# Performance work log

Hardware: AMD Instinct MI355X
Metric: run time of the kernel (lower is better)

Reference implementation:

```python
import jax, jax.numpy as jnp
import numpy as np

C, H, V, N, T = 256, 256, 10000, 8, 256


def _residual_mlp(x, w1, b1, w2, b2, w3, b3):
    # ResidualLayerOld: relu(lin2(relu(lin1(x)))) + x, then final Linear
    h = jax.nn.relu(x @ w1 + b1)
    h = jax.nn.relu(h @ w2 + b2) + x
    return h @ w3 + b3


def setup_inputs() -> dict:
    key = jax.random.key(0)
    ks = jax.random.split(key, 16)
    p = lambda k, shape: jax.random.normal(k, shape, jnp.float32) * 0.02
    return dict(
        text=jax.random.randint(ks[0], (N, T), 0, V),
        mask=jnp.ones((N, T), dtype=bool),
        lengths=jnp.full((N,), T - 1, dtype=jnp.int32),  # full-length sequences
        start_emb=jax.random.normal(ks[1], (C, H), jnp.float32),
        state_emb=jax.random.normal(ks[2], (C, H), jnp.float32),
        preterminal_emb=jax.random.normal(ks[3], (C, H), jnp.float32),
        start_w1=p(ks[4], (H, H)), start_b1=jnp.zeros((H,), jnp.float32),
        start_w2=p(ks[5], (H, H)), start_b2=jnp.zeros((H,), jnp.float32),
        start_w3=p(ks[6], (H, 1)), start_b3=jnp.zeros((1,), jnp.float32),
        trans_w1=p(ks[7], (H, H)), trans_b1=jnp.zeros((H,), jnp.float32),
        trans_w2=p(ks[8], (H, H)), trans_b2=jnp.zeros((H,), jnp.float32),
        trans_w3=p(ks[9], (H, C)), trans_b3=jnp.zeros((C,), jnp.float32),
        term_w1=p(ks[10], (H, H)), term_b1=jnp.zeros((H,), jnp.float32),
        term_w2=p(ks[11], (H, H)), term_b2=jnp.zeros((H,), jnp.float32),
        term_w3=p(ks[12], (H, V)), term_b3=jnp.zeros((V,), jnp.float32),
    )


def _score(text, mask, lengths,
           start_emb, state_emb, preterminal_emb,
           start_w1, start_b1, start_w2, start_b2, start_w3, start_b3,
           trans_w1, trans_b1, trans_w2, trans_b2, trans_w3, trans_b3,
           term_w1, term_b1, term_w2, term_b2, term_w3, term_b3):
    n, t = text.shape
    c = state_emb.shape[0]
    # start / transition / emission distributions (dropout_type == 'none')
    init = jax.nn.log_softmax(
        _residual_mlp(start_emb, start_w1, start_b1, start_w2, start_b2, start_w3, start_b3)[:, 0], -1)  # [C]
    trans = jax.nn.log_softmax(
        _residual_mlp(state_emb, trans_w1, trans_b1, trans_w2, trans_b2, trans_w3, trans_b3), -1)  # [C,C]
    log_em = jax.nn.log_softmax(
        _residual_mlp(preterminal_emb, term_w1, term_b1, term_w2, term_b2, term_w3, term_b3), -1)  # [C,V]
    obs = log_em.T[text]  # [N,T,C], log p(x_t | z=c)
    # torch_struct LinearChain.hmm edge potentials: phi[n,t,c_next,c_prev]
    phi = trans[None, None] + obs[:, 1:, :, None]  # [N,T-1,C,C]
    phi = phi.at[:, 0].add(init[None, None, :] + obs[:, 0][:, None, :])
    phi_t = jnp.swapaxes(phi, 0, 1)  # [T-1,N,C,C]

    def fwd_step(alpha, p):
        new = jax.nn.logsumexp(p + alpha[:, None, :], axis=-1)  # reduce over c_prev
        return new, new

    _, alphas = jax.lax.scan(fwd_step, jnp.zeros((n, c), phi.dtype), phi_t)  # [T-1,N,C]

    def bwd_step(beta, p):
        new = jax.nn.logsumexp(p + beta[:, :, None], axis=1)  # reduce over c_next
        return new, beta

    _, betas = jax.lax.scan(bwd_step, jnp.zeros((n, c), phi.dtype), phi_t, reverse=True)  # [T-1,N,C]

    alpha_prev = jnp.concatenate([jnp.zeros((1, n, c), phi.dtype), alphas[:-1]], 0)
    log_Z = jax.nn.logsumexp(alphas[-1], -1)  # [N]
    # edge posteriors
    log_m = alpha_prev[:, :, None, :] + phi_t + betas[:, :, :, None] - log_Z[None, :, None, None]
    marginals = jnp.swapaxes(jnp.exp(log_m), 0, 1)  # [N,T-1,C,C]

    evidence = jax.nn.logsumexp(alphas[lengths - 1, jnp.arange(n)], -1).sum()
    elbo = jnp.where(mask[:, 1:, None, None],
                     jax.lax.stop_gradient(marginals) * phi,
                     0.0).sum()
    return elbo, evidence


def reference(text, mask, lengths,
              start_emb, state_emb, preterminal_emb,
              start_w1, start_b1, start_w2, start_b2, start_w3, start_b3,
              trans_w1, trans_b1, trans_w2, trans_b2, trans_w3, trans_b3,
              term_w1, term_b1, term_w2, term_b2, term_w3, term_b3):
    elbo, evidence = _score(text, mask, lengths,
                            start_emb, state_emb, preterminal_emb,
                            start_w1, start_b1, start_w2, start_b2, start_w3, start_b3,
                            trans_w1, trans_b1, trans_w2, trans_b2, trans_w3, trans_b3,
                            term_w1, term_b1, term_w2, term_b2, term_w3, term_b3)
    return elbo, evidence
```

## Files before the change

kernel.cpp:

```cpp
#include <hip/hip_runtime.h>
#include <hip/hip_bf16.h>

#define C_ 256
#define H_ 256
#define V_ 10000
#define N_ 8
#define T_ 256
#define TM1_ 255
#define NB_ ((V_ + 31) / 32)
#define SW_ 8

typedef _Float16 h2_t __attribute__((ext_vector_type(2)));
typedef _Float16 h4_t __attribute__((ext_vector_type(4)));
typedef _Float16 h8_t __attribute__((ext_vector_type(8)));
typedef float f4v __attribute__((ext_vector_type(4)));

__device__ __forceinline__ void bar_lgkm() {
  asm volatile("s_waitcnt lgkmcnt(0)\ns_barrier" ::: "memory");
}

__device__ __forceinline__ float wave_red_max(float v) {
#define DPP_MAX(ctrl) { int iv_ = __float_as_int(v); \
  int r_ = __builtin_amdgcn_update_dpp(iv_, iv_, ctrl, 0xF, 0xF, false); \
  v = fmaxf(v, __int_as_float(r_)); }
// ... 37 lines not shown
  const int tid = threadIdx.x;
#pragma unroll
  for (int rr = 0; rr < 4; ++rr)
    e_s[rr][tid] = emb[(r0 + rr) * H_ + tid];
  __syncthreads();
  float bb = b1[tid];
  float a0 = bb, a1 = bb, a2 = bb, a3 = bb;
  for (int k4 = 0; k4 < H_ / 4; ++k4) {
    float4 e0 = ((const float4*)e_s[0])[k4];
    float4 e1 = ((const float4*)e_s[1])[k4];
    float4 e2 = ((const float4*)e_s[2])[k4];
    float4 e3 = ((const float4*)e_s[3])[k4];
    const float* wp = w1 + (k4 * 4) * H_ + tid;
    float wa = wp[0], wb = wp[H_], wc = wp[2 * H_], wd = wp[3 * H_];
    a0 = fmaf(e0.x, wa, a0); a0 = fmaf(e0.y, wb, a0);
    a0 = fmaf(e0.z, wc, a0); a0 = fmaf(e0.w, wd, a0);
    a1 = fmaf(e1.x, wa, a1); a1 = fmaf(e1.y, wb, a1);
    a1 = fmaf(e1.z, wc, a1); a1 = fmaf(e1.w, wd, a1);
    a2 = fmaf(e2.x, wa, a2); a2 = fmaf(e2.y, wb, a2);
    a2 = fmaf(e2.z, wc, a2); a2 = fmaf(e2.w, wd, a2);
    a3 = fmaf(e3.x, wa, a3); a3 = fmaf(e3.y, wb, a3);
    a3 = fmaf(e3.z, wc, a3); a3 = fmaf(e3.w, wd, a3);
  }
  h_s[0][tid] = fmaxf(a0, 0.f);
  h_s[1][tid] = fmaxf(a1, 0.f);
  h_s[2][tid] = fmaxf(a2, 0.f);
  h_s[3][tid] = fmaxf(a3, 0.f);
  __syncthreads();
  bb = b2[tid];
  a0 = bb; a1 = bb; a2 = bb; a3 = bb;
  for (int k4 = 0; k4 < H_ / 4; ++k4) {
    float4 e0 = ((const float4*)h_s[0])[k4];
    float4 e1 = ((const float4*)h_s[1])[k4];
    float4 e2 = ((const float4*)h_s[2])[k4];
    float4 e3 = ((const float4*)h_s[3])[k4];
    const float* wp = w2 + (k4 * 4) * H_ + tid;
    float wa = wp[0], wb = wp[H_], wc = wp[2 * H_], wd = wp[3 * H_];
    a0 = fmaf(e0.x, wa, a0); a0 = fmaf(e0.y, wb, a0);
    a0 = fmaf(e0.z, wc, a0); a0 = fmaf(e0.w, wd, a0);
    a1 = fmaf(e1.x, wa, a1); a1 = fmaf(e1.y, wb, a1);
    a1 = fmaf(e1.z, wc, a1); a1 = fmaf(e1.w, wd, a1);
    a2 = fmaf(e2.x, wa, a2); a2 = fmaf(e2.y, wb, a2);
    a2 = fmaf(e2.z, wc, a2); a2 = fmaf(e2.w, wd, a2);
    a3 = fmaf(e3.x, wa, a3); a3 = fmaf(e3.y, wb, a3);
    a3 = fmaf(e3.z, wc, a3); a3 = fmaf(e3.w, wd, a3);
  }
  h2_s[0][tid] = fmaxf(a0, 0.f) + e_s[0][tid];
  h2_s[1][tid] = fmaxf(a1, 0.f) + e_s[1][tid];
  h2_s[2][tid] = fmaxf(a2, 0.f) + e_s[2][tid];
  h2_s[3][tid] = fmaxf(a3, 0.f) + e_s[3][tid];
  __syncthreads();
}

__global__ __launch_bounds__(256) void k_start(
    const float* __restrict__ emb, const float* __restrict__ w1,
    const float* __restrict__ b1, const float* __restrict__ w2,
    const float* __restrict__ b2, const float* __restrict__ w3,
    const float* __restrict__ b3, float* __restrict__ slogit) {
  __shared__ __align__(16) float e_s[4][C_], h_s[4][C_], h2_s[4][C_];
  __shared__ float red[4];
  const int r0 = blockIdx.x * 4;
  const int tid = threadIdx.x;
  mlp4(emb, w1, b1, w2, b2, r0, e_s, h_s, h2_s);
  float w3v = w3[tid];
  float s0 = block_allsum(h2_s[0][tid] * w3v, red);
  float s1 = block_allsum(h2_s[1][tid] * w3v, red);
  float s2 = block_allsum(h2_s[2][tid] * w3v, red);
  float s3 = block_allsum(h2_s[3][tid] * w3v, red);
  if (tid == 0) {
    float bb = b3[0];
    slogit[r0 + 0] = s0 + bb;
    slogit[r0 + 1] = s1 + bb;
    slogit[r0 + 2] = s2 + bb;
    slogit[r0 + 3] = s3 + bb;
  }
}

__global__ void k_init(const float* __restrict__ slogit, float* __restrict__ initv) {
  __shared__ float red[4];
  const int tid = threadIdx.x;
  float x = slogit[tid];
  float m = block_allmax(x, red);
  float se = block_allsum(__expf(x - m), red);
  initv[tid] = x - m - __logf(se);
}

__global__ __launch_bounds__(256) void k_trans(
    const float* __restrict__ emb, const float* __restrict__ w1,
    const float* __restrict__ b1, const float* __restrict__ w2,
    const float* __restrict__ b2, const float* __restrict__ w3,
    const float* __restrict__ b3, float* __restrict__ Pf,
    float* __restrict__ PLf, float* __restrict__ PTf,
    _Float16* __restrict__ P_h, _Float16* __restrict__ PT_h) {
  __shared__ __align__(16) float e_s[4][C_], h_s[4][C_], h2_s[4][C_];
  __shared__ float red[4];
  const int r0 = blockIdx.x * 4;
  const int tid = threadIdx.x;
  mlp4(emb, w1, b1, w2, b2, r0, e_s, h_s, h2_s);
  float lb = b3[tid];
  float l0 = lb, l1 = lb, l2 = lb, l3 = lb;
  for (int k4 = 0; k4 < H_ / 4; ++k4) {
    float4 e0 = ((const float4*)h2_s[0])[k4];
    float4 e1 = ((const float4*)h2_s[1])[k4];
    float4 e2 = ((const float4*)h2_s[2])[k4];
    float4 e3 = ((const float4*)h2_s[3])[k4];
    const float* wp = w3 + (k4 * 4) * C_ + tid;
    float wa = wp[0], wb = wp[C_], wc = wp[2 * C_], wd = wp[3 * C_];
    l0 = fmaf(e0.x, wa, l0); l0 = fmaf(e0.y, wb, l0);
    l0 = fmaf(e0.z, wc, l0); l0 = fmaf(e0.w, wd, l0);
    l1 = fmaf(e1.x, wa, l1); l1 = fmaf(e1.y, wb, l1);
    l1 = fmaf(e1.z, wc, l1); l1 = fmaf(e1.w, wd, l1);
    l2 = fmaf(e2.x, wa, l2); l2 = fmaf(e2.y, wb, l2);
    l2 = fmaf(e2.z, wc, l2); l2 = fmaf(e2.w, wd, l2);
    l3 = fmaf(e3.x, wa, l3); l3 = fmaf(e3.y, wb, l3);
    l3 = fmaf(e3.z, wc, l3); l3 = fmaf(e3.w, wd, l3);
  }
  float lg[4] = {l0, l1, l2, l3};
#pragma unroll
  for (int rr = 0; rr < 4; ++rr) {
    float m = block_allmax(lg[rr], red);
    float e = __expf(lg[rr] - m);
    float se = block_allsum(e, red);
    float p = e / se;
    float tv = lg[rr] - m - __logf(se);
    const int r = r0 + rr;
    Pf[r * C_ + tid] = p;
    PLf[r * C_ + tid] = p * tv;
    PTf[tid * C_ + r] = p;
    P_h[r * C_ + tid] = (_Float16)p;
    PT_h[tid * C_ + r] = (_Float16)p;
  }
}

__global__ __launch_bounds__(256) void k_term_mlp(
    const float* __restrict__ emb, const float* __restrict__ w1,
    const float* __restrict__ b1, const float* __restrict__ w2,
    const float* __restrict__ b2, float* __restrict__ H2,
    float* __restrict__ H2T) {
  __shared__ __align__(16) float e_s[4][C_], h_s[4][C_], h2_s[4][C_];
  const int r0 = blockIdx.x * 4;
  const int tid = threadIdx.x;
  mlp4(emb, w1, b1, w2, b2, r0, e_s, h_s, h2_s);
#pragma unroll
  for (int rr = 0; rr < 4; ++rr) {
    const int r = r0 + rr;
    float v = h2_s[rr][tid];
    H2[r * H_ + tid] = v;
    H2T[tid * C_ + r] = v;
  }
}

__global__ __launch_bounds__(256) void k_term_stats(
    const float* __restrict__ H2, const float* __restrict__ w3,
    const float* __restrict__ b3, float* __restrict__ partm,
    float* __restrict__ parts) {
  __shared__ __align__(16) float w3_s[H_][32];
  __shared__ float b3_s[32];
  const int v0 = blockIdx.x * 32;
  const int tid = threadIdx.x;
  const int ncols = min(32, V_ - v0);
  for (int idx = tid; idx < H_ * 32; idx += 256) {
    int k = idx >> 5, c = idx & 31;
    w3_s[k][c] = (c < ncols) ? w3[k * V_ + v0 + c] : 0.f;
  }
  if (tid < 32) b3_s[tid] = (tid < ncols) ? b3[v0 + tid] : 0.f;
  __syncthreads();
  float acc[32];
#pragma unroll
  for (int c = 0; c < 32; ++c) acc[c] = 0.f;
  const float4* hq = (const float4*)(H2 + tid * H_);
  for (int k4 = 0; k4 < H_ / 4; ++k4) {
    float4 h = hq[k4];
    float hk[4];
    *(float4*)hk = h;
#pragma unroll
    for (int kk = 0; kk < 4; ++kk) {
      float hv = hk[kk];
      const int k = k4 * 4 + kk;
      const float4* wq = (const float4*)(&w3_s[k][0]);
#pragma unroll
      for (int c4 = 0; c4 < 8; ++c4) {
        float4 w = wq[c4];
        acc[c4 * 4 + 0] = fmaf(hv, w.x, acc[c4 * 4 + 0]);
        acc[c4 * 4 + 1] = fmaf(hv, w.y, acc[c4 * 4 + 1]);
        acc[c4 * 4 + 2] = fmaf(hv, w.z, acc[c4 * 4 + 2]);
        acc[c4 * 4 + 3] = fmaf(hv, w.w, acc[c4 * 4 + 3]);
      }
    }
  }
  float m = -1e30f;
#pragma unroll
  for (int c = 0; c < 32; ++c) {
    acc[c] += b3_s[c];
    if (c < ncols) m = fmaxf(m, acc[c]);
  }
  float se = 0.f;
#pragma unroll
  for (int c = 0; c < 32; ++c)
    if (c < ncols) se += __expf(acc[c] - m);
  partm[blockIdx.x * C_ + tid] = m;
  parts[blockIdx.x * C_ + tid] = se;
}

__global__ void k_denom(const float* __restrict__ partm,
                        const float* __restrict__ parts,
                        float* __restrict__ denom) {
  const int r = threadIdx.x;
  float m = -1e30f;
  for (int b = 0; b < NB_; ++b) m = fmaxf(m, partm[b * C_ + r]);
  float s = 0.f;
  for (int b = 0; b < NB_; ++b)
    s += parts[b * C_ + r] * __expf(partm[b * C_ + r] - m);
  denom[r] = m + __logf(s);
}

__global__ __launch_bounds__(256) void k_obs2(
    const int* __restrict__ text, const float* __restrict__ H2T,
    const float* __restrict__ w3, const float* __restrict__ b3,
    const float* __restrict__ denom, float* __restrict__ EOBS,
    float* __restrict__ Karr) {
  __shared__ __align__(16) float w_s[H_][8];
  __shared__ float redm[4][8];
  const int c = threadIdx.x;
  const int wid = c >> 6;
  const int lane = c & 63;
  const int base = blockIdx.x * 8;
  int tok[8];
#pragma unroll
  for (int i = 0; i < 8; ++i) tok[i] = text[base + i];
  float wtmp[8];
#pragma unroll
  for (int i = 0; i < 8; ++i) wtmp[i] = w3[c * V_ + tok[i]];
  float b3t[8];
#pragma unroll
  for (int i = 0; i < 8; ++i) b3t[i] = b3[tok[i]];
#pragma unroll
  for (int i = 0; i < 8; ++i) w_s[c][i] = wtmp[i];
  __syncthreads();
  float acc[8];
#pragma unroll
  for (int i = 0; i < 8; ++i) acc[i] = 0.f;
  for (int k4 = 0; k4 < H_ / 4; ++k4) {
    float hv[4];
#pragma unroll
    for (int kk = 0; kk < 4; ++kk) hv[kk] = H2T[(k4 * 4 + kk) * C_ + c];
#pragma unroll
    for (int kk = 0; kk < 4; ++kk) {
      const float4* wq = (const float4*)(&w_s[k4 * 4 + kk][0]);
      float4 wa = wq[0], wb = wq[1];
      acc[0] = fmaf(hv[kk], wa.x, acc[0]);
      acc[1] = fmaf(hv[kk], wa.y, acc[1]);
      acc[2] = fmaf(hv[kk], wa.z, acc[2]);
      acc[3] = fmaf(hv[kk], wa.w, acc[3]);
      acc[4] = fmaf(hv[kk], wb.x, acc[4]);
      acc[5] = fmaf(hv[kk], wb.y, acc[5]);
      acc[6] = fmaf(hv[kk], wb.z, acc[6]);
      acc[7] = fmaf(hv[kk], wb.w, acc[7]);
    }
  }
  float dn = denom[c];
  float obsv[8];
#pragma unroll
  for (int i = 0; i < 8; ++i) obsv[i] = acc[i] + b3t[i] - dn;
#pragma unroll
  for (int i = 0; i < 8; ++i) {
    float wm = wave_red_max(obsv[i]);
    if (lane == 0) redm[wid][i] = wm;
  }
  __syncthreads();
#pragma unroll
  for (int i = 0; i < 8; ++i) {
    float Ki = fmaxf(fmaxf(redm[0][i], redm[1][i]),
                     fmaxf(redm[2][i], redm[3][i]));
    EOBS[(base + i) * C_ + c] = __expf(obsv[i] - Ki);
    if (c == 0) Karr[base + i] = Ki;
  }
}

__global__ __launch_bounds__(512, 2) void k_scan5(
    const _Float16* __restrict__ P_h, const _Float16* __restrict__ PT_h,
    const float* __restrict__ initv, const float* __restrict__ EOBS,
    const float* __restrict__ Karr, float* __restrict__ AL,
    float* __restrict__ BL, float* __restrict__ CC, float* __restrict__ DD,
    float* __restrict__ LOGZ) {
  __shared__ __align__(16) _Float16 ubuf[2][C_];
  __shared__ __align__(16) float red[SW_];
  const int tid = threadIdx.x;
  const int w = tid >> 6;
  const int lane = tid & 63;
  const int quad = lane >> 4;
  const int nn16 = lane & 15;
  const bool bwd = blockIdx.x >= N_;
  const int n = blockIdx.x & (N_ - 1);
  const _Float16* __restrict__ M = bwd ? PT_h : P_h;

  h8_t afrag[2][8];
#pragma unroll
  for (int m = 0; m < 2; ++m) {
    const _Float16* rp = M + (size_t)((w << 5) + (m << 4) + nn16) * C_ + (quad << 3);
#pragma unroll
    for (int kt = 0; kt < 8; ++kt)
      afrag[m][kt] = *(const h8_t*)(rp + (kt << 5));
  }
  const int stb = (w << 5) + (quad << 2);

  if (!bwd) {
    float K0 = Karr[n * T_];
    f4v x0[2];
    float lmax = -1e30f;
#pragma unroll
    for (int m = 0; m < 2; ++m) {
      const int st0 = stb + (m << 4);
      f4v iv = *(const f4v*)(initv + st0);
      f4v e0 = *(const f4v*)(EOBS + (size_t)(n * T_) * C_ + st0);
#pragma unroll
      for (int r = 0; r < 4; ++r) {
        x0[m][r] = iv[r] + __logf(e0[r]) + K0;
        lmax = fmaxf(lmax, x0[m][r]);
      }
    }
    float wmx = wave_red_max(lmax);
    if (lane == 0) red[w] = wmx;
    __syncthreads();
    f4v rr0 = *(const f4v*)&red[0];
    f4v rr1 = *(const f4v*)&red[4];
    float m0 = fmaxf(fmaxf(fmaxf(rr0[0], rr0[1]), fmaxf(rr0[2], rr0[3])),
                     fmaxf(fmaxf(rr1[0], rr1[1]), fmaxf(rr1[2], rr1[3])));
    __syncthreads();
    float Cacc = m0;
    f4v uval[2];
#pragma unroll
    for (int m = 0; m < 2; ++m) {
      const int st0 = stb + (m << 4);
#pragma unroll
      for (int r = 0; r < 4; ++r) uval[m][r] = __expf(x0[m][r] - m0);
      if (nn16 == 0) {
        h4_t p;
#pragma unroll
        for (int r = 0; r < 4; ++r) p[r] = (_Float16)uval[m][r];
        *(h4_t*)(&ubuf[0][st0]) = p;
        *(f4v*)(AL + (size_t)(0 * N_ + n) * C_ + st0) = uval[m];
      }
    }
    if (tid == 0) CC[0 * N_ + n] = Cacc;
    float invm = 1.f, logm = 0.f;
    f4v eo_nx[2], eo_p1[2];
#pragma unroll
    for (int m = 0; m < 2; ++m) {
      eo_nx[m] = *(const f4v*)(EOBS + (size_t)(n * T_ + 1) * C_ + stb + (m << 4));
      eo_p1[m] = *(const f4v*)(EOBS + (size_t)(n * T_ + 2) * C_ + stb + (m << 4));
    }
    float K_nx = Karr[n * T_ + 1];
    float K_p1 = Karr[n * T_ + 2];
    __syncthreads();

#pragma unroll 1
    for (int t = 0; t < TM1_; ++t) {
      const int cur = t & 1, nxt = cur ^ 1;
      f4v eo_p2[2];
      float K_p2 = 0.f;
      if (t + 3 < T_) {
#pragma unroll
        for (int m = 0; m < 2; ++m)
          eo_p2[m] = *(const f4v*)(EOBS + (size_t)(n * T_ + t + 3) * C_ + stb + (m << 4));
        K_p2 = Karr[n * T_ + t + 3];
      }
      h8_t bf[8];
#pragma unroll
      for (int kt = 0; kt < 8; ++kt)
        bf[kt] = *(const h8_t*)(&ubuf[cur][(kt << 5) + (quad << 3)]);
      f4v acc[2];
      acc[0] = (f4v){0.f, 0.f, 0.f, 0.f};
      acc[1] = (f4v){0.f, 0.f, 0.f, 0.f};
#pragma unroll
      for (int kt = 0; kt < 8; ++kt) {
        acc[0] = __builtin_amdgcn_mfma_f32_16x16x32_f16(afrag[0][kt], bf[kt], acc[0], 0, 0, 0);
        acc[1] = __builtin_amdgcn_mfma_f32_16x16x32_f16(afrag[1][kt], bf[kt], acc[1], 0, 0, 0);
      }
      float lmx = -1e30f;
#pragma unroll
      for (int m = 0; m < 2; ++m) {
#pragma unroll
        for (int r = 0; r < 4; ++r) {
          float u = acc[m][r] * invm * eo_nx[m][r];
          uval[m][r] = u;
          lmx = fmaxf(lmx, u);
        }
      }
      Cacc += K_nx + logm;
      const bool resc = (t & 3) == 3;
      if (resc) {
        float wmm = wave_red_max(lmx);
        if (lane == 0) red[w] = wmm;
      }
      if (nn16 == 0) {
#pragma unroll
        for (int m = 0; m < 2; ++m) {
          const int st0 = stb + (m << 4);
          h4_t p;
#pragma unroll
          for (int r = 0; r < 4; ++r) p[r] = (_Float16)uval[m][r];
          *(h4_t*)(&ubuf[nxt][st0]) = p;
          *(f4v*)(AL + (size_t)((t + 1) * N_ + n) * C_ + st0) = uval[m];
        }
      }
      if (tid == 0) CC[(t + 1) * N_ + n] = Cacc;
      bar_lgkm();
      if (resc) {
        f4v q0 = *(const f4v*)&red[0];
        f4v q1 = *(const f4v*)&red[4];
        float mm = fmaxf(fmaxf(fmaxf(q0[0], q0[1]), fmaxf(q0[2], q0[3])),
                         fmaxf(fmaxf(q1[0], q1[1]), fmaxf(q1[2], q1[3])));
        mm = fmaxf(mm, 1e-30f);
        invm = 1.f / mm;
        logm = __logf(mm);
      } else { invm = 1.f; logm = 0.f; }
#pragma unroll
      for (int m = 0; m < 2; ++m) { eo_nx[m] = eo_p1[m]; eo_p1[m] = eo_p2[m]; }
      K_nx = K_p1; K_p1 = K_p2;
    }
    float s = 0.f;
#pragma unroll
    for (int m = 0; m < 2; ++m)
      s += (uval[m][0] + uval[m][1]) + (uval[m][2] + uval[m][3]);
    s = wave_red_sum(s);
    if (lane == 0) red[w] = s;
    __syncthreads();
    if (tid == 0) {
      float S = ((red[0] + red[1]) + (red[2] + red[3])) +
                ((red[4] + red[5]) + (red[6] + red[7]));
      LOGZ[n] = __logf(S * (1.f / 16.f)) + Cacc;
    }
  } else {
    float Dacc = 0.f;
    f4v vval[2];
#pragma unroll
    for (int m = 0; m < 2; ++m) {
      const int st0 = stb + (m << 4);
      vval[m] = *(const f4v*)(EOBS + ((size_t)n * T_ + TM1_) * C_ + st0);
      if (nn16 == 0) {
        h4_t p;
#pragma unroll
        for (int r = 0; r < 4; ++r) p[r] = (_Float16)vval[m][r];
        *(h4_t*)(&ubuf[0][st0]) = p;
        f4v one = (f4v){1.f, 1.f, 1.f, 1.f};
        *(f4v*)(BL + (size_t)((TM1_ - 1) * N_ + n) * C_ + st0) = one;
      }
    }
    if (tid == 0) DD[(TM1_ - 1) * N_ + n] = 0.f;
    float K_nx = Karr[n * T_ + TM1_];
    float K_p1 = Karr[n * T_ + TM1_ - 1];
    f4v eo_nx[2], eo_p1[2];
#pragma unroll
    for (int m = 0; m < 2; ++m) {
      eo_nx[m] = *(const f4v*)(EOBS + (size_t)(n * T_ + TM1_ - 1) * C_ + stb + (m << 4));
      eo_p1[m] = *(const f4v*)(EOBS + (size_t)(n * T_ + TM1_ - 2) * C_ + stb + (m << 4));
    }
    float invm = 1.f, logm = 0.f;
    __syncthreads();

#pragma unroll 1
    for (int it = 0, t = TM1_ - 2; t >= 0; --t, ++it) {
      const int cur = it & 1, nxt = cur ^ 1;
      f4v eo_p2[2];
      float K_p2 = 0.f;
      if (t >= 2) {
#pragma unroll
        for (int m = 0; m < 2; ++m)
          eo_p2[m] = *(const f4v*)(EOBS + (size_t)(n * T_ + t - 1) * C_ + stb + (m << 4));
        K_p2 = Karr[n * T_ + t];
      }
      h8_t bf[8];
#pragma unroll
      for (int kt = 0; kt < 8; ++kt)
        bf[kt] = *(const h8_t*)(&ubuf[cur][(kt << 5) + (quad << 3)]);
      f4v acc[2];
      acc[0] = (f4v){0.f, 0.f, 0.f, 0.f};
      acc[1] = (f4v){0.f, 0.f, 0.f, 0.f};
#pragma unroll
      for (int kt = 0; kt < 8; ++kt) {
        acc[0] = __builtin_amdgcn_mfma_f32_16x16x32_f16(afrag[0][kt], bf[kt], acc[0], 0, 0, 0);
        acc[1] = __builtin_amdgcn_mfma_f32_16x16x32_f16(afrag[1][kt], bf[kt], acc[1], 0, 0, 0);
      }
      Dacc += K_nx + logm;
      float lmx = -1e30f;
      f4v blv[2];
#pragma unroll
      for (int m = 0; m < 2; ++m) {
#pragma unroll
        for (int r = 0; r < 4; ++r) {
          float b = acc[m][r] * invm;
          blv[m][r] = b;
          float v = b * eo_nx[m][r];
          vval[m][r] = v;
          lmx = fmaxf(lmx, v);
        }
      }
      if (((it + 1) & 3) == 3) {
        float wmm = wave_red_max(lmx);
        if (lane == 0) red[w] = wmm;
      }
      if (nn16 == 0) {
#pragma unroll
        for (int m = 0; m < 2; ++m) {
          const int st0 = stb + (m << 4);
          h4_t p;
#pragma unroll
          for (int r = 0; r < 4; ++r) p[r] = (_Float16)vval[m][r];
          *(h4_t*)(&ubuf[nxt][st0]) = p;
          *(f4v*)(BL + (size_t)(t * N_ + n) * C_ + st0) = blv[m];
        }
      }
      if (tid == 0) DD[t * N_ + n] = Dacc;
      bar_lgkm();
      if (((it + 1) & 3) == 3) {
        f4v q0 = *(const f4v*)&red[0];
        f4v q1 = *(const f4v*)&red[4];
        float mm = fmaxf(fmaxf(fmaxf(q0[0], q0[1]), fmaxf(q0[2], q0[3])),
                         fmaxf(fmaxf(q1[0], q1[1]), fmaxf(q1[2], q1[3])));
        mm = fmaxf(mm, 1e-30f);
        invm = 1.f / mm;
        logm = __logf(mm);
      } else { invm = 1.f; logm = 0.f; }
#pragma unroll
      for (int m = 0; m < 2; ++m) { eo_nx[m] = eo_p1[m]; eo_p1[m] = eo_p2[m]; }
      K_nx = K_p1; K_p1 = K_p2;
    }
  }
}

__global__ __launch_bounds__(256) void k_elbo(
    const float* __restrict__ Pf, const float* __restrict__ PLf,
    const float* __restrict__ PTf, const float* __restrict__ AL,
    const float* __restrict__ BL, const float* __restrict__ CC,
    const float* __restrict__ DD, const float* __restrict__ EOBS,
    const float* __restrict__ Karr, const float* __restrict__ LOGZ,
    float* __restrict__ out) {
  __shared__ __align__(16) float A_s[N_][C_];
  __shared__ __align__(16) float B_s[N_][C_];
  __shared__ float red[4];
  const int t = blockIdx.x;
  const int c = threadIdx.x;
  if (t == 0 && c == 0) {
    float s = 0.f;
#pragma unroll
    for (int nn = 0; nn < N_; ++nn) s += LOGZ[nn];
    out[1] = s;
  }
  float sc[N_], Kv[N_], cc[N_];
#pragma unroll
  for (int nn = 0; nn < N_; ++nn) {
    A_s[nn][c] = AL[(t * N_ + nn) * C_ + c];
    Kv[nn] = Karr[nn * T_ + t + 1];
    cc[nn] = CC[t * N_ + nn];
    sc[nn] = __expf(cc[nn] + DD[t * N_ + nn] + Kv[nn] - LOGZ[nn]);
  }
  __syncthreads();
  float accPA[N_], accPL[N_];
#pragma unroll
  for (int nn = 0; nn < N_; ++nn) { accPA[nn] = 0.f; accPL[nn] = 0.f; }
  const float4* pr = (const float4*)(Pf + c * C_);
  const float4* plr = (const float4*)(PLf + c * C_);
  for (int j = 0; j < C_ / 4; ++j) {
    float4 p = pr[j];
    float4 pl = plr[j];
#pragma unroll
    for (int nn = 0; nn < N_; ++nn) {
      float4 a = ((const float4*)A_s[nn])[j];
      accPA[nn] += p.x * a.x + p.y * a.y + p.z * a.z + p.w * a.w;
      accPL[nn] += pl.x * a.x + pl.y * a.y + pl.z * a.z + pl.w * a.w;
    }
  }
  float contrib = 0.f;
  float Bv[N_];
#pragma unroll
  for (int nn = 0; nn < N_; ++nn) {
    float eo = EOBS[(nn * T_ + t + 1) * C_ + c];
    float ob = __logf(eo) + Kv[nn];
    float B = eo * BL[(t * N_ + nn) * C_ + c] * sc[nn];
    Bv[nn] = B;
    contrib += B * fmaf(ob, accPA[nn], accPL[nn]);
  }
  if (t == 0) {
#pragma unroll
    for (int nn = 0; nn < N_; ++nn) B_s[nn][c] = Bv[nn];
    __syncthreads();
    const float4* ptq = (const float4*)(PTf + c * C_);
    float accPT[N_];
#pragma unroll
    for (int nn = 0; nn < N_; ++nn) accPT[nn] = 0.f;
    for (int j = 0; j < C_ / 4; ++j) {
      float4 p = ptq[j];
#pragma unroll
      for (int nn = 0; nn < N_; ++nn) {
        float4 b = ((const float4*)B_s[nn])[j];
        accPT[nn] += p.x * b.x + p.y * b.y + p.z * b.z + p.w * b.w;
      }
    }
#pragma unroll
    for (int nn = 0; nn < N_; ++nn) {
      float a0v = A_s[nn][c];
      if (a0v > 0.f)
        contrib += a0v * (__logf(a0v) + cc[nn]) * accPT[nn];
    }
  }
  contrib = wave_red_sum(contrib);
  if ((c & 63) == 0) red[c >> 6] = contrib;
  __syncthreads();
  if (c == 0) atomicAdd(out, (red[0] + red[1]) + (red[2] + red[3]));
}

extern "C" void kernel_launch(void* const* d_in, const int* in_sizes, int n_in,
                              void* d_out, int out_size, void* d_ws, size_t ws_size,
                              hipStream_t stream) {
  (void)in_sizes; (void)n_in; (void)out_size; (void)ws_size;
  const int* text = (const int*)d_in[0];
  const float* start_emb = (const float*)d_in[3];
  const float* state_emb = (const float*)d_in[4];
  const float* pre_emb   = (const float*)d_in[5];
  const float* sw1 = (const float*)d_in[6];  const float* sb1 = (const float*)d_in[7];
  const float* sw2 = (const float*)d_in[8];  const float* sb2 = (const float*)d_in[9];
  const float* sw3 = (const float*)d_in[10]; const float* sb3 = (const float*)d_in[11];
  const float* tw1 = (const float*)d_in[12]; const float* tb1 = (const float*)d_in[13];
  const float* tw2 = (const float*)d_in[14]; const float* tb2 = (const float*)d_in[15];
  const float* tw3 = (const float*)d_in[16]; const float* tb3 = (const float*)d_in[17];
  const float* ew1 = (const float*)d_in[18]; const float* eb1 = (const float*)d_in[19];
  const float* ew2 = (const float*)d_in[20]; const float* eb2 = (const float*)d_in[21];
  const float* ew3 = (const float*)d_in[22]; const float* eb3 = (const float*)d_in[23];
  float* out = (float*)d_out;

  char* p = (char*)d_ws;
  auto alloc = [&](size_t bytes) -> char* {
    char* r = p;
    p += (bytes + 255) & ~(size_t)255;
    return r;
  };
  float* slogit = (float*)alloc(C_ * 4);
  float* initv  = (float*)alloc(C_ * 4);
  float* denom  = (float*)alloc(C_ * 4);
  float* LOGZ   = (float*)alloc(N_ * 4);
  float* Pf     = (float*)alloc(C_ * C_ * 4);
  float* PLf    = (float*)alloc(C_ * C_ * 4);
  float* PTf    = (float*)alloc(C_ * C_ * 4);
  _Float16* P_h  = (_Float16*)alloc(C_ * C_ * 2);
  _Float16* PT_h = (_Float16*)alloc(C_ * C_ * 2);
  float* H2    = (float*)alloc(C_ * H_ * 4);
  float* H2T   = (float*)alloc(C_ * H_ * 4);
  float* partm = (float*)alloc(NB_ * C_ * 4);
  float* parts = (float*)alloc(NB_ * C_ * 4);
  float* EOBS  = (float*)alloc((size_t)N_ * T_ * C_ * 4);
  float* Karr  = (float*)alloc((size_t)N_ * T_ * 4);
  float* AL    = (float*)alloc((size_t)T_ * N_ * C_ * 4);
  float* BL    = (float*)alloc((size_t)TM1_ * N_ * C_ * 4);
  float* CC    = (float*)alloc((size_t)T_ * N_ * 4);
  float* DD    = (float*)alloc((size_t)TM1_ * N_ * 4);

  hipMemsetAsync(d_out, 0, 2 * sizeof(float), stream);

  k_start<<<dim3(C_ / 4), dim3(256), 0, stream>>>(start_emb, sw1, sb1, sw2, sb2, sw3, sb3, slogit);
  k_init<<<dim3(1), dim3(256), 0, stream>>>(slogit, initv);
  k_trans<<<dim3(C_ / 4), dim3(256), 0, stream>>>(state_emb, tw1, tb1, tw2, tb2, tw3, tb3,
                                                  Pf, PLf, PTf, P_h, PT_h);
  k_term_mlp<<<dim3(C_ / 4), dim3(256), 0, stream>>>(pre_emb, ew1, eb1, ew2, eb2, H2, H2T);
  k_term_stats<<<dim3(NB_), dim3(256), 0, stream>>>(H2, ew3, eb3, partm, parts);
  k_denom<<<dim3(1), dim3(256), 0, stream>>>(partm, parts, denom);
  k_obs2<<<dim3(N_ * T_ / 8), dim3(256), 0, stream>>>(text, H2T, ew3, eb3, denom, EOBS, Karr);
  k_scan5<<<dim3(2 * N_), dim3(512), 0, stream>>>(P_h, PT_h, initv, EOBS, Karr,
                                                  AL, BL, CC, DD, LOGZ);
  k_elbo<<<dim3(TM1_), dim3(256), 0, stream>>>(Pf, PLf, PTf, AL, BL, CC, DD,
                                               EOBS, Karr, LOGZ, out);
}
```

Measured before the change: 517.0 us.

## Fuse head MLP kernels, merge small reductions, unroll scan with rotating prefetch slots

Merges the start, transition and terminal MLP kernels into one 192-block launch, and merges the init log-softmax and denominator kernels into a single two-block launch, cutting launch count and serial dependencies. The forward/backward scan is unrolled by three with rotating register slots for prefetched emission rows, removing the per-step register shuffling. The per-step K scaling terms are taken out of the scan and replaced by a total K sum computed once up front, which is passed to the final kernel. The extra block-level reduction adds a small prologue to the scan, and the merged kernels carry more divergent code per block.

```diff
diff --git a/kernel.cpp b/kernel.cpp
--- a/kernel.cpp
+++ b/kernel.cpp
@@ -113,101 +113,86 @@
   __syncthreads();
 }
 
-__global__ __launch_bounds__(256) void k_start(
-    const float* __restrict__ emb, const float* __restrict__ w1,
-    const float* __restrict__ b1, const float* __restrict__ w2,
-    const float* __restrict__ b2, const float* __restrict__ w3,
-    const float* __restrict__ b3, float* __restrict__ slogit) {
+__global__ __launch_bounds__(256) void k_heads(
+    const float* __restrict__ semb, const float* __restrict__ sw1,
+    const float* __restrict__ sb1, const float* __restrict__ sw2,
+    const float* __restrict__ sb2, const float* __restrict__ sw3,
+    const float* __restrict__ sb3, float* __restrict__ slogit,
+    const float* __restrict__ temb, const float* __restrict__ tw1,
+    const float* __restrict__ tb1, const float* __restrict__ tw2,
+    const float* __restrict__ tb2, const float* __restrict__ tw3,
+    const float* __restrict__ tb3, float* __restrict__ Pf,
+    float* __restrict__ PLf, float* __restrict__ PTf,
+    _Float16* __restrict__ P_h, _Float16* __restrict__ PT_h,
+    const float* __restrict__ eemb, const float* __restrict__ ew1,
+    const float* __restrict__ eb1, const float* __restrict__ ew2,
+    const float* __restrict__ eb2, float* __restrict__ H2,
+    float* __restrict__ H2T) {
   __shared__ __align__(16) float e_s[4][C_], h_s[4][C_], h2_s[4][C_];
   __shared__ float red[4];
-  const int r0 = blockIdx.x * 4;
+  const int b = blockIdx.x;
   const int tid = threadIdx.x;
-  mlp4(emb, w1, b1, w2, b2, r0, e_s, h_s, h2_s);
-  float w3v = w3[tid];
-  float s0 = block_allsum(h2_s[0][tid] * w3v, red);
-  float s1 = block_allsum(h2_s[1][tid] * w3v, red);
-  float s2 = block_allsum(h2_s[2][tid] * w3v, red);
-  float s3 = block_allsum(h2_s[3][tid] * w3v, red);
-  if (tid == 0) {
-    float bb = b3[0];
-    slogit[r0 + 0] = s0 + bb;
-    slogit[r0 + 1] = s1 + bb;
-    slogit[r0 + 2] = s2 + bb;
-    slogit[r0 + 3] = s3 + bb;
-  }
-}
-
-__global__ void k_init(const float* __restrict__ slogit, float* __restrict__ initv) {
-  __shared__ float red[4];
-  const int tid = threadIdx.x;
-  float x = slogit[tid];
-  float m = block_allmax(x, red);
-  float se = block_allsum(__expf(x - m), red);
-  initv[tid] = x - m - __logf(se);
-}
-
-__global__ __launch_bounds__(256) void k_trans(
-    const float* __restrict__ emb, const float* __restrict__ w1,
-    const float* __restrict__ b1, const float* __restrict__ w2,
-    const float* __restrict__ b2, const float* __restrict__ w3,
-    const float* __restrict__ b3, float* __restrict__ Pf,
-    float* __restrict__ PLf, float* __restrict__ PTf,
-    _Float16* __restrict__ P_h, _Float16* __restrict__ PT_h) {
-  __shared__ __align__(16) float e_s[4][C_], h_s[4][C_], h2_s[4][C_];
-  __shared__ float red[4];
-  const int r0 = blockIdx.x * 4;
-  const int tid = threadIdx.x;
-  mlp4(emb, w1, b1, w2, b2, r0, e_s, h_s, h2_s);
-  float lb = b3[tid];
-  float l0 = lb, l1 = lb, l2 = lb, l3 = lb;
-  for (int k4 = 0; k4 < H_ / 4; ++k4) {
-    float4 e0 = ((const float4*)h2_s[0])[k4];
-    float4 e1 = ((const float4*)h2_s[1])[k4];
-    float4 e2 = ((const float4*)h2_s[2])[k4];
-    float4 e3 = ((const float4*)h2_s[3])[k4];
-    const float* wp = w3 + (k4 * 4) * C_ + tid;
-    float wa = wp[0], wb = wp[C_], wc = wp[2 * C_], wd = wp[3 * C_];
-    l0 = fmaf(e0.x, wa, l0); l0 = fmaf(e0.y, wb, l0);
-    l0 = fmaf(e0.z, wc, l0); l0 = fmaf(e0.w, wd, l0);
-    l1 = fmaf(e1.x, wa, l1); l1 = fmaf(e1.y, wb, l1);
-    l1 = fmaf(e1.z, wc, l1); l1 = fmaf(e1.w, wd, l1);
-    l2 = fmaf(e2.x, wa, l2); l2 = fmaf(e2.y, wb, l2);
-    l2 = fmaf(e2.z, wc, l2); l2 = fmaf(e2.w, wd, l2);
-    l3 = fmaf(e3.x, wa, l3); l3 = fmaf(e3.y, wb, l3);
-    l3 = fmaf(e3.z, wc, l3); l3 = fmaf(e3.w, wd, l3);
-  }
-  float lg[4] = {l0, l1, l2, l3};
-#pragma unroll
-  for (int rr = 0; rr < 4; ++rr) {
-    float m = block_allmax(lg[rr], red);
-    float e = __expf(lg[rr] - m);
-    float se = block_allsum(e, red);
-    float p = e / se;
-    float tv = lg[rr] - m - __logf(se);
-    const int r = r0 + rr;
-    Pf[r * C_ + tid] = p;
-    PLf[r * C_ + tid] = p * tv;
-    PTf[tid * C_ + r] = p;
-    P_h[r * C_ + tid] = (_Float16)p;
-    PT_h[tid * C_ + r] = (_Float16)p;
-  }
-}
-
-__global__ __launch_bounds__(256) void k_term_mlp(
-    const float* __restrict__ emb, const float* __restrict__ w1,
-    const float* __restrict__ b1, const float* __restrict__ w2,
-    const float* __restrict__ b2, float* __restrict__ H2,
-    float* __restrict__ H2T) {
-  __shared__ __align__(16) float e_s[4][C_], h_s[4][C_], h2_s[4][C_];
-  const int r0 = blockIdx.x * 4;
-  const int tid = threadIdx.x;
-  mlp4(emb, w1, b1, w2, b2, r0, e_s, h_s, h2_s);
-#pragma unroll
-  for (int rr = 0; rr < 4; ++rr) {
-    const int r = r0 + rr;
-    float v = h2_s[rr][tid];
-    H2[r * H_ + tid] = v;
-    H2T[tid * C_ + r] = v;
+  if (b < 64) {
+    const int r0 = b * 4;
+    mlp4(semb, sw1, sb1, sw2, sb2, r0, e_s, h_s, h2_s);
+    float w3v = sw3[tid];
+    float s0 = block_allsum(h2_s[0][tid] * w3v, red);
+    float s1 = block_allsum(h2_s[1][tid] * w3v, red);
+    float s2 = block_allsum(h2_s[2][tid] * w3v, red);
+    float s3 = block_allsum(h2_s[3][tid] * w3v, red);
+    if (tid == 0) {
+      float bb = sb3[0];
+      slogit[r0 + 0] = s0 + bb;
+      slogit[r0 + 1] = s1 + bb;
+      slogit[r0 + 2] = s2 + bb;
+      slogit[r0 + 3] = s3 + bb;
+    }
+  } else if (b < 128) {
+    const int r0 = (b - 64) * 4;
+    mlp4(temb, tw1, tb1, tw2, tb2, r0, e_s, h_s, h2_s);
+    float lb = tb3[tid];
+    float l0 = lb, l1 = lb, l2 = lb, l3 = lb;
+    for (int k4 = 0; k4 < H_ / 4; ++k4) {
+      float4 e0 = ((const float4*)h2_s[0])[k4];
+      float4 e1 = ((const float4*)h2_s[1])[k4];
+      float4 e2 = ((const float4*)h2_s[2])[k4];
+      float4 e3 = ((const float4*)h2_s[3])[k4];
+      const float* wp = tw3 + (k4 * 4) * C_ + tid;
+      float wa = wp[0], wb = wp[C_], wc = wp[2 * C_], wd = wp[3 * C_];
+      l0 = fmaf(e0.x, wa, l0); l0 = fmaf(e0.y, wb, l0);
+      l0 = fmaf(e0.z, wc, l0); l0 = fmaf(e0.w, wd, l0);
+      l1 = fmaf(e1.x, wa, l1); l1 = fmaf(e1.y, wb, l1);
+      l1 = fmaf(e1.z, wc, l1); l1 = fmaf(e1.w, wd, l1);
+      l2 = fmaf(e2.x, wa, l2); l2 = fmaf(e2.y, wb, l2);
+      l2 = fmaf(e2.z, wc, l2); l2 = fmaf(e2.w, wd, l2);
+      l3 = fmaf(e3.x, wa, l3); l3 = fmaf(e3.y, wb, l3);
+      l3 = fmaf(e3.z, wc, l3); l3 = fmaf(e3.w, wd, l3);
+    }
+    float lg[4] = {l0, l1, l2, l3};
+#pragma unroll
+    for (int rr = 0; rr < 4; ++rr) {
+      float m = block_allmax(lg[rr], red);
+      float e = __expf(lg[rr] - m);
+      float se = block_allsum(e, red);
+      float p = e / se;
+      float tv = lg[rr] - m - __logf(se);
+      const int r = r0 + rr;
+      Pf[r * C_ + tid] = p;
+      PLf[r * C_ + tid] = p * tv;
+      PTf[tid * C_ + r] = p;
+      P_h[r * C_ + tid] = (_Float16)p;
+      PT_h[tid * C_ + r] = (_Float16)p;
+    }
+  } else {
+    const int r0 = (b - 128) * 4;
+    mlp4(eemb, ew1, eb1, ew2, eb2, r0, e_s, h_s, h2_s);
+#pragma unroll
+    for (int rr = 0; rr < 4; ++rr) {
+      const int r = r0 + rr;
+      float v = h2_s[rr][tid];
+      H2[r * H_ + tid] = v;
+      H2T[tid * C_ + r] = v;
+    }
   }
 }
 
@@ -263,16 +248,27 @@
   parts[blockIdx.x * C_ + tid] = se;
 }
 
-__global__ void k_denom(const float* __restrict__ partm,
+__global__ void k_small(const float* __restrict__ slogit,
+                        float* __restrict__ initv,
+                        const float* __restrict__ partm,
                         const float* __restrict__ parts,
                         float* __restrict__ denom) {
-  const int r = threadIdx.x;
-  float m = -1e30f;
-  for (int b = 0; b < NB_; ++b) m = fmaxf(m, partm[b * C_ + r]);
-  float s = 0.f;
-  for (int b = 0; b < NB_; ++b)
-    s += parts[b * C_ + r] * __expf(partm[b * C_ + r] - m);
-  denom[r] = m + __logf(s);
+  __shared__ float red[4];
+  const int tid = threadIdx.x;
+  if (blockIdx.x == 0) {
+    float x = slogit[tid];
+    float m = block_allmax(x, red);
+    float se = block_allsum(__expf(x - m), red);
+    initv[tid] = x - m - __logf(se);
+  } else {
+    const int r = tid;
+    float m = -1e30f;
+    for (int b = 0; b < NB_; ++b) m = fmaxf(m, partm[b * C_ + r]);
+    float s = 0.f;
+    for (int b = 0; b < NB_; ++b)
+      s += parts[b * C_ + r] * __expf(partm[b * C_ + r] - m);
+    denom[r] = m + __logf(s);
+  }
 }
 
 __global__ __launch_bounds__(256) void k_obs2(
@@ -338,12 +334,12 @@
   }
 }
 
-__global__ __launch_bounds__(512, 2) void k_scan5(
+__global__ __launch_bounds__(512, 2) void k_scan6(
     const _Float16* __restrict__ P_h, const _Float16* __restrict__ PT_h,
     const float* __restrict__ initv, const float* __restrict__ EOBS,
     const float* __restrict__ Karr, float* __restrict__ AL,
     float* __restrict__ BL, float* __restrict__ CC, float* __restrict__ DD,
-    float* __restrict__ LOGZ) {
+    float* __restrict__ KT, float* __restrict__ LOGZ) {
   __shared__ __align__(16) _Float16 ubuf[2][C_];
   __shared__ __align__(16) float red[SW_];
   const int tid = threadIdx.x;
@@ -364,8 +360,24 @@
       afrag[m][kt] = *(const h8_t*)(rp + (kt << 5));
   }
   const int stb = (w << 5) + (quad << 2);
+  const float* __restrict__ eob = EOBS + (size_t)n * T_ * C_;
+  int cur = 0;
+
+  f4v eoA[2], eoB[2], eoC[2];
+#define FLOAD(SL, tt) { \
+  eo##SL[0] = *(const f4v*)(eob + (size_t)(tt) * C_ + stb); \
+  eo##SL[1] = *(const f4v*)(eob + (size_t)(tt) * C_ + stb + 16); }
 
   if (!bwd) {
+    float kvp = (tid >= 1 && tid < 256) ? Karr[n * T_ + tid] : 0.f;
+    kvp = wave_red_sum(kvp);
+    if (lane == 0) red[w] = kvp;
+    __syncthreads();
+    float KPtot = ((red[0] + red[1]) + (red[2] + red[3])) +
+                  ((red[4] + red[5]) + (red[6] + red[7]));
+    if (tid == 0) KT[n] = KPtot;
+    __syncthreads();
+
     float K0 = Karr[n * T_];
     f4v x0[2];
     float lmax = -1e30f;
@@ -373,7 +385,7 @@
     for (int m = 0; m < 2; ++m) {
       const int st0 = stb + (m << 4);
       f4v iv = *(const f4v*)(initv + st0);
-      f4v e0 = *(const f4v*)(EOBS + (size_t)(n * T_) * C_ + st0);
+      f4v e0 = *(const f4v*)(eob + st0);
 #pragma unroll
       for (int r = 0; r < 4; ++r) {
         x0[m][r] = iv[r] + __logf(e0[r]) + K0;
@@ -388,7 +400,7 @@
     float m0 = fmaxf(fmaxf(fmaxf(rr0[0], rr0[1]), fmaxf(rr0[2], rr0[3])),
                      fmaxf(fmaxf(rr1[0], rr1[1]), fmaxf(rr1[2], rr1[3])));
     __syncthreads();
-    float Cacc = m0;
+    float CLacc = m0;
     f4v uval[2];
 #pragma unroll
     for (int m = 0; m < 2; ++m) {
@@ -403,83 +415,61 @@
         *(f4v*)(AL + (size_t)(0 * N_ + n) * C_ + st0) = uval[m];
       }
     }
-    if (tid == 0) CC[0 * N_ + n] = Cacc;
+    if (tid == 0) CC[0 * N_ + n] = CLacc;
     float invm = 1.f, logm = 0.f;
-    f4v eo_nx[2], eo_p1[2];
-#pragma unroll
-    for (int m = 0; m < 2; ++m) {
-      eo_nx[m] = *(const f4v*)(EOBS + (size_t)(n * T_ + 1) * C_ + stb + (m << 4));
-      eo_p1[m] = *(const f4v*)(EOBS + (size_t)(n * T_ + 2) * C_ + stb + (m << 4));
-    }
-    float K_nx = Karr[n * T_ + 1];
-    float K_p1 = Karr[n * T_ + 2];
+    FLOAD(B, 1)
+    FLOAD(C, 2)
     __syncthreads();
 
+#define FSTEP(tt, SL, SC) do { \
+    if ((tt) + 3 < T_) FLOAD(SL, (tt) + 3) \
+    const _Float16* ubc = &ubuf[cur][0]; \
+    _Float16* ubn = &ubuf[cur ^ 1][0]; \
+    h8_t bf[8]; \
+    _Pragma("unroll") for (int kt = 0; kt < 8; ++kt) \
+      bf[kt] = *(const h8_t*)(ubc + (kt << 5) + (quad << 3)); \
+    f4v acc0 = (f4v){0.f, 0.f, 0.f, 0.f}; \
+    f4v acc1 = (f4v){0.f, 0.f, 0.f, 0.f}; \
+    _Pragma("unroll") for (int kt = 0; kt < 8; ++kt) { \
+      acc0 = __builtin_amdgcn_mfma_f32_16x16x32_f16(afrag[0][kt], bf[kt], acc0, 0, 0, 0); \
+      acc1 = __builtin_amdgcn_mfma_f32_16x16x32_f16(afrag[1][kt], bf[kt], acc1, 0, 0, 0); } \
+    float lmx = -1e30f; \
+    _Pragma("unroll") for (int r = 0; r < 4; ++r) { \
+      uval[0][r] = acc0[r] * invm * eo##SC[0][r]; lmx = fmaxf(lmx, uval[0][r]); \
+      uval[1][r] = acc1[r] * invm * eo##SC[1][r]; lmx = fmaxf(lmx, uval[1][r]); } \
+    CLacc += logm; \
+    const bool resc_ = ((tt) & 3) == 3; \
+    if (resc_) { \
+      float wmm = wave_red_max(lmx); \
+      if (lane == 0) red[w] = wmm; } \
+    if (nn16 == 0) { \
+      _Pragma("unroll") for (int m = 0; m < 2; ++m) { \
+        const int st0 = stb + (m << 4); \
+        h4_t p; \
+        _Pragma("unroll") for (int r = 0; r < 4; ++r) p[r] = (_Float16)uval[m][r]; \
+        *(h4_t*)(ubn + st0) = p; \
+        *(f4v*)(AL + (size_t)(((tt) + 1) * N_ + n) * C_ + st0) = uval[m]; } } \
+    if (tid == 0) CC[((tt) + 1) * N_ + n] = CLacc; \
+    bar_lgkm(); \
+    if (resc_) { \
+      f4v q0 = *(const f4v*)&red[0]; \
+      f4v q1 = *(const f4v*)&red[4]; \
+      float mm = fmaxf(fmaxf(fmaxf(q0[0], q0[1]), fmaxf(q0[2], q0[3])), \
+                       fmaxf(fmaxf(q1[0], q1[1]), fmaxf(q1[2], q1[3]))); \
+      mm = fmaxf(mm, 1e-30f); \
+      invm = 1.f / mm; \
+      logm = __logf(mm); \
+    } else { invm = 1.f; logm = 0.f; } \
+    cur ^= 1; \
+  } while (0)
+
 #pragma unroll 1
-    for (int t = 0; t < TM1_; ++t) {
-      const int cur = t & 1, nxt = cur ^ 1;
-      f4v eo_p2[2];
-      float K_p2 = 0.f;
-      if (t + 3 < T_) {
-#pragma unroll
-        for (int m = 0; m < 2; ++m)
-          eo_p2[m] = *(const f4v*)(EOBS + (size_t)(n * T_ + t + 3) * C_ + stb + (m << 4));
-        K_p2 = Karr[n * T_ + t + 3];
-      }
-      h8_t bf[8];
-#pragma unroll
-      for (int kt = 0; kt < 8; ++kt)
-        bf[kt] = *(const h8_t*)(&ubuf[cur][(kt << 5) + (quad << 3)]);
-      f4v acc[2];
-      acc[0] = (f4v){0.f, 0.f, 0.f, 0.f};
-      acc[1] = (f4v){0.f, 0.f, 0.f, 0.f};
-#pragma unroll
-      for (int kt = 0; kt < 8; ++kt) {
-        acc[0] = __builtin_amdgcn_mfma_f32_16x16x32_f16(afrag[0][kt], bf[kt], acc[0], 0, 0, 0);
-        acc[1] = __builtin_amdgcn_mfma_f32_16x16x32_f16(afrag[1][kt], bf[kt], acc[1], 0, 0, 0);
-      }
-      float lmx = -1e30f;
-#pragma unroll
-      for (int m = 0; m < 2; ++m) {
-#pragma unroll
-        for (int r = 0; r < 4; ++r) {
-          float u = acc[m][r] * invm * eo_nx[m][r];
-          uval[m][r] = u;
-          lmx = fmaxf(lmx, u);
-        }
-      }
-      Cacc += K_nx + logm;
-      const bool resc = (t & 3) == 3;
-      if (resc) {
-        float wmm = wave_red_max(lmx);
-        if (lane == 0) red[w] = wmm;
-      }
-      if (nn16 == 0) {
-#pragma unroll
-        for (int m = 0; m < 2; ++m) {
-          const int st0 = stb + (m << 4);
-          h4_t p;
-#pragma unroll
-          for (int r = 0; r < 4; ++r) p[r] = (_Float16)uval[m][r];
-          *(h4_t*)(&ubuf[nxt][st0]) = p;
-          *(f4v*)(AL + (size_t)((t + 1) * N_ + n) * C_ + st0) = uval[m];
-        }
-      }
-      if (tid == 0) CC[(t + 1) * N_ + n] = Cacc;
-      bar_lgkm();
-      if (resc) {
-        f4v q0 = *(const f4v*)&red[0];
-        f4v q1 = *(const f4v*)&red[4];
-        float mm = fmaxf(fmaxf(fmaxf(q0[0], q0[1]), fmaxf(q0[2], q0[3])),
-                         fmaxf(fmaxf(q1[0], q1[1]), fmaxf(q1[2], q1[3])));
-        mm = fmaxf(mm, 1e-30f);
-        invm = 1.f / mm;
-        logm = __logf(mm);
-      } else { invm = 1.f; logm = 0.f; }
-#pragma unroll
-      for (int m = 0; m < 2; ++m) { eo_nx[m] = eo_p1[m]; eo_p1[m] = eo_p2[m]; }
-      K_nx = K_p1; K_p1 = K_p2;
-    }
+    for (int tb = 0; tb < TM1_; tb += 3) {
+      FSTEP(tb + 0, A, B);
+      FSTEP(tb + 1, B, C);
+      FSTEP(tb + 2, C, A);
+    }
+#undef FSTEP
     float s = 0.f;
 #pragma unroll
     for (int m = 0; m < 2; ++m)
@@ -490,15 +480,15 @@
     if (tid == 0) {
       float S = ((red[0] + red[1]) + (red[2] + red[3])) +
                 ((red[4] + red[5]) + (red[6] + red[7]));
-      LOGZ[n] = __logf(S * (1.f / 16.f)) + Cacc;
+      LOGZ[n] = __logf(S * (1.f / 16.f)) + CLacc + KPtot;
     }
   } else {
-    float Dacc = 0.f;
+    float DLacc = 0.f;
     f4v vval[2];
 #pragma unroll
     for (int m = 0; m < 2; ++m) {
       const int st0 = stb + (m << 4);
-      vval[m] = *(const f4v*)(EOBS + ((size_t)n * T_ + TM1_) * C_ + st0);
+      vval[m] = *(const f4v*)(eob + (size_t)TM1_ * C_ + st0);
       if (nn16 == 0) {
         h4_t p;
 #pragma unroll
@@ -509,85 +499,66 @@
       }
     }
     if (tid == 0) DD[(TM1_ - 1) * N_ + n] = 0.f;
-    float K_nx = Karr[n * T_ + TM1_];
-    float K_p1 = Karr[n * T_ + TM1_ - 1];
-    f4v eo_nx[2], eo_p1[2];
-#pragma unroll
-    for (int m = 0; m < 2; ++m) {
-      eo_nx[m] = *(const f4v*)(EOBS + (size_t)(n * T_ + TM1_ - 1) * C_ + stb + (m << 4));
-      eo_p1[m] = *(const f4v*)(EOBS + (size_t)(n * T_ + TM1_ - 2) * C_ + stb + (m << 4));
-    }
-    float invm = 1.f, logm = 0.f;
+    FLOAD(B, TM1_ - 1)
+    FLOAD(C, TM1_ - 2)
     __syncthreads();
 
+#define BSTEP(itv, SL, SC) do { \
+    if ((itv) < TM1_ - 1) { \
+      const int t_ = TM1_ - 2 - (itv); \
+      if ((itv) <= TM1_ - 4) FLOAD(SL, t_ - 1) \
+      float invm = 1.f, logm = 0.f; \
+      if (((itv) & 3) == 3) { \
+        f4v q0 = *(const f4v*)&red[0]; \
+        f4v q1 = *(const f4v*)&red[4]; \
+        float mm = fmaxf(fmaxf(fmaxf(q0[0], q0[1]), fmaxf(q0[2], q0[3])), \
+                         fmaxf(fmaxf(q1[0], q1[1]), fmaxf(q1[2], q1[3]))); \
+        mm = fmaxf(mm, 1e-30f); \
+        invm = 1.f / mm; \
+        logm = __logf(mm); } \
+      const _Float16* ubc = &ubuf[cur][0]; \
+      _Float16* ubn = &ubuf[cur ^ 1][0]; \
+      h8_t bf[8]; \
+      _Pragma("unroll") for (int kt = 0; kt < 8; ++kt) \
+        bf[kt] = *(const h8_t*)(ubc + (kt << 5) + (quad << 3)); \
+      f4v acc0 = (f4v){0.f, 0.f, 0.f, 0.f}; \
+      f4v acc1 = (f4v){0.f, 0.f, 0.f, 0.f}; \
+      _Pragma("unroll") for (int kt = 0; kt < 8; ++kt) { \
+        acc0 = __builtin_amdgcn_mfma_f32_16x16x32_f16(afrag[0][kt], bf[kt], acc0, 0, 0, 0); \
+        acc1 = __builtin_amdgcn_mfma_f32_16x16x32_f16(afrag[1][kt], bf[kt], acc1, 0, 0, 0); } \
+      DLacc += logm; \
+      float lmx = -1e30f; \
+      f4v blv[2]; \
+      _Pragma("unroll") for (int r = 0; r < 4; ++r) { \
+        blv[0][r] = acc0[r] * invm; \
+        vval[0][r] = blv[0][r] * eo##SC[0][r]; lmx = fmaxf(lmx, vval[0][r]); \
+        blv[1][r] = acc1[r] * invm; \
+        vval[1][r] = blv[1][r] * eo##SC[1][r]; lmx = fmaxf(lmx, vval[1][r]); } \
+      if ((((itv) + 1) & 3) == 3) { \
+        float wmm = wave_red_max(lmx); \
+        if (lane == 0) red[w] = wmm; } \
+      if (nn16 == 0) { \
+        _Pragma("unroll") for (int m = 0; m < 2; ++m) { \
+          const int st0 = stb + (m << 4); \
+          h4_t p; \
+          _Pragma("unroll") for (int r = 0; r < 4; ++r) p[r] = (_Float16)vval[m][r]; \
+          *(h4_t*)(ubn + st0) = p; \
+          *(f4v*)(BL + (size_t)(t_ * N_ + n) * C_ + st0) = blv[m]; } } \
+      if (tid == 0) DD[t_ * N_ + n] = DLacc; \
+      bar_lgkm(); \
+      cur ^= 1; \
+    } \
+  } while (0)
+
 #pragma unroll 1
-    for (int it = 0, t = TM1_ - 2; t >= 0; --t, ++it) {
-      const int cur = it & 1, nxt = cur ^ 1;
-      f4v eo_p2[2];
-      float K_p2 = 0.f;
-      if (t >= 2) {
-#pragma unroll
-        for (int m = 0; m < 2; ++m)
-          eo_p2[m] = *(const f4v*)(EOBS + (size_t)(n * T_ + t - 1) * C_ + stb + (m << 4));
-        K_p2 = Karr[n * T_ + t];
-      }
-      h8_t bf[8];
-#pragma unroll
-      for (int kt = 0; kt < 8; ++kt)
-        bf[kt] = *(const h8_t*)(&ubuf[cur][(kt << 5) + (quad << 3)]);
-      f4v acc[2];
-      acc[0] = (f4v){0.f, 0.f, 0.f, 0.f};
-      acc[1] = (f4v){0.f, 0.f, 0.f, 0.f};
-#pragma unroll
-      for (int kt = 0; kt < 8; ++kt) {
-        acc[0] = __builtin_amdgcn_mfma_f32_16x16x32_f16(afrag[0][kt], bf[kt], acc[0], 0, 0, 0);
-        acc[1] = __builtin_amdgcn_mfma_f32_16x16x32_f16(afrag[1][kt], bf[kt], acc[1], 0, 0, 0);
-      }
-      Dacc += K_nx + logm;
-      float lmx = -1e30f;
-      f4v blv[2];
-#pragma unroll
-      for (int m = 0; m < 2; ++m) {
-#pragma unroll
-        for (int r = 0; r < 4; ++r) {
-          float b = acc[m][r] * invm;
-          blv[m][r] = b;
-          float v = b * eo_nx[m][r];
-          vval[m][r] = v;
-          lmx = fmaxf(lmx, v);
-        }
-      }
-      if (((it + 1) & 3) == 3) {
-        float wmm = wave_red_max(lmx);
-        if (lane == 0) red[w] = wmm;
-      }
-      if (nn16 == 0) {
-#pragma unroll
-        for (int m = 0; m < 2; ++m) {
-          const int st0 = stb + (m << 4);
-          h4_t p;
-#pragma unroll
-          for (int r = 0; r < 4; ++r) p[r] = (_Float16)vval[m][r];
-          *(h4_t*)(&ubuf[nxt][st0]) = p;
-          *(f4v*)(BL + (size_t)(t * N_ + n) * C_ + st0) = blv[m];
-        }
-      }
-      if (tid == 0) DD[t * N_ + n] = Dacc;
-      bar_lgkm();
-      if (((it + 1) & 3) == 3) {
-        f4v q0 = *(const f4v*)&red[0];
-        f4v q1 = *(const f4v*)&red[4];
-        float mm = fmaxf(fmaxf(fmaxf(q0[0], q0[1]), fmaxf(q0[2], q0[3])),
-                         fmaxf(fmaxf(q1[0], q1[1]), fmaxf(q1[2], q1[3])));
-        mm = fmaxf(mm, 1e-30f);
-        invm = 1.f / mm;
-        logm = __logf(mm);
-      } else { invm = 1.f; logm = 0.f; }
-#pragma unroll
-      for (int m = 0; m < 2; ++m) { eo_nx[m] = eo_p1[m]; eo_p1[m] = eo_p2[m]; }
-      K_nx = K_p1; K_p1 = K_p2;
-    }
-  }
+    for (int ib = 0; ib < 255; ib += 3) {
+      BSTEP(ib + 0, A, B);
+      BSTEP(ib + 1, B, C);
+      BSTEP(ib + 2, C, A);
+    }
+#undef BSTEP
+  }
+#undef FLOAD
 }
 
 __global__ __launch_bounds__(256) void k_elbo(
@@ -595,8 +566,8 @@
     const float* __restrict__ PTf, const float* __restrict__ AL,
     const float* __restrict__ BL, const float* __restrict__ CC,
     const float* __restrict__ DD, const float* __restrict__ EOBS,
-    const float* __restrict__ Karr, const float* __restrict__ LOGZ,
-    float* __restrict__ out) {
+    const float* __restrict__ Karr, const float* __restrict__ KT,
+    const float* __restrict__ LOGZ, float* __restrict__ out) {
   __shared__ __align__(16) float A_s[N_][C_];
   __shared__ __align__(16) float B_s[N_][C_];
   __shared__ float red[4];
@@ -614,7 +585,7 @@
     A_s[nn][c] = AL[(t * N_ + nn) * C_ + c];
     Kv[nn] = Karr[nn * T_ + t + 1];
     cc[nn] = CC[t * N_ + nn];
-    sc[nn] = __expf(cc[nn] + DD[t * N_ + nn] + Kv[nn] - LOGZ[nn]);
+    sc[nn] = __expf(cc[nn] + DD[t * N_ + nn] + KT[nn] - LOGZ[nn]);
   }
   __syncthreads();
   float accPA[N_], accPL[N_];
@@ -700,6 +671,7 @@
   float* initv  = (float*)alloc(C_ * 4);
   float* denom  = (float*)alloc(C_ * 4);
   float* LOGZ   = (float*)alloc(N_ * 4);
+  float* KT     = (float*)alloc(N_ * 4);
   float* Pf     = (float*)alloc(C_ * C_ * 4);
   float* PLf    = (float*)alloc(C_ * C_ * 4);
   float* PTf    = (float*)alloc(C_ * C_ * 4);
@@ -718,16 +690,15 @@
 
   hipMemsetAsync(d_out, 0, 2 * sizeof(float), stream);
 
-  k_start<<<dim3(C_ / 4), dim3(256), 0, stream>>>(start_emb, sw1, sb1, sw2, sb2, sw3, sb3, slogit);
-  k_init<<<dim3(1), dim3(256), 0, stream>>>(slogit, initv);
-  k_trans<<<dim3(C_ / 4), dim3(256), 0, stream>>>(state_emb, tw1, tb1, tw2, tb2, tw3, tb3,
-                                                  Pf, PLf, PTf, P_h, PT_h);
-  k_term_mlp<<<dim3(C_ / 4), dim3(256), 0, stream>>>(pre_emb, ew1, eb1, ew2, eb2, H2, H2T);
+  k_heads<<<dim3(192), dim3(256), 0, stream>>>(
+      start_emb, sw1, sb1, sw2, sb2, sw3, sb3, slogit,
+      state_emb, tw1, tb1, tw2, tb2, tw3, tb3, Pf, PLf, PTf, P_h, PT_h,
+      pre_emb, ew1, eb1, ew2, eb2, H2, H2T);
   k_term_stats<<<dim3(NB_), dim3(256), 0, stream>>>(H2, ew3, eb3, partm, parts);
-  k_denom<<<dim3(1), dim3(256), 0, stream>>>(partm, parts, denom);
+  k_small<<<dim3(2), dim3(256), 0, stream>>>(slogit, initv, partm, parts, denom);
   k_obs2<<<dim3(N_ * T_ / 8), dim3(256), 0, stream>>>(text, H2T, ew3, eb3, denom, EOBS, Karr);
-  k_scan5<<<dim3(2 * N_), dim3(512), 0, stream>>>(P_h, PT_h, initv, EOBS, Karr,
-                                                  AL, BL, CC, DD, LOGZ);
+  k_scan6<<<dim3(2 * N_), dim3(512), 0, stream>>>(P_h, PT_h, initv, EOBS, Karr,
+                                                  AL, BL, CC, DD, KT, LOGZ);
   k_elbo<<<dim3(TM1_), dim3(256), 0, stream>>>(Pf, PLf, PTf, AL, BL, CC, DD,
-                                               EOBS, Karr, LOGZ, out);
-}
+                                               EOBS, Karr, KT, LOGZ, out);
+}
```

Result: faster. 467.7 us (median of 3 runs) (-9.5%).
